# Performance work log

Measured on AMD Instinct MI355X. Metric: run time of the kernel, lower is better.

Reference implementation:

```python
import jax, jax.numpy as jnp
import numpy as np

D_MODEL = 1024
N_HEADS = 16
D_HEAD = D_MODEL // N_HEADS


def setup_inputs() -> dict:
    key = jax.random.key(0)
    ks = jax.random.split(key, 5)
    B, T = 2, 2048
    x = jax.random.normal(ks[0], (B, T, D_MODEL), dtype=jnp.float32)
    # Linear weights stored as [in, out]; scale ~ nn.Linear default magnitude
    W_qkv = jax.random.normal(ks[1], (D_MODEL, 3 * D_MODEL), dtype=jnp.float32) * (1.0 / np.sqrt(D_MODEL))
    b_qkv = jnp.zeros((3 * D_MODEL,), dtype=jnp.float32)
    W_out = jax.random.normal(ks[2], (D_MODEL, D_MODEL), dtype=jnp.float32) * (1.0 / np.sqrt(D_MODEL))
    b_out = jnp.zeros((D_MODEL,), dtype=jnp.float32)
    return {"x": x, "W_qkv": W_qkv, "b_qkv": b_qkv, "W_out": W_out, "b_out": b_out}


def reference(x, W_qkv, b_qkv, W_out, b_out):
    B, T, C = x.shape
    H, Dh = N_HEADS, D_HEAD
    qkv = x @ W_qkv + b_qkv                     # [B, T, 3C]
    q, k, v = jnp.split(qkv, 3, axis=-1)
    # [B, H, T, Dh]
    q = q.reshape(B, T, H, Dh).transpose(0, 2, 1, 3)
    k = k.reshape(B, T, H, Dh).transpose(0, 2, 1, 3)
    v = v.reshape(B, T, H, Dh).transpose(0, 2, 1, 3)
    att = jnp.einsum('bhqd,bhkd->bhqk', q, k) / np.sqrt(Dh).astype(np.float32)
    causal = jnp.tril(jnp.ones((T, T), dtype=bool))  # [T, T]
    att = jnp.where(causal[None, None], att, jnp.float32(-1e9))
    att = jax.nn.softmax(att, axis=-1)
    y = jnp.einsum('bhqk,bhkd->bhqd', att, v)   # [B, H, T, Dh]
    y = y.transpose(0, 2, 1, 3).reshape(B, T, C)
    y = y @ W_out + b_out
    return (y, k, v)  # y plus present KV cache
```

## Files before the change

kernel.cpp:

```cpp
#include <hip/hip_runtime.h>

typedef __attribute__((ext_vector_type(8))) short bf16x8;
typedef __attribute__((ext_vector_type(4))) float f32x4;
typedef __attribute__((ext_vector_type(16))) float f32x16;

#define MFMA16(A, B, C) __builtin_amdgcn_mfma_f32_16x16x32_bf16((A), (B), (C), 0, 0, 0)
#define MFMA32(A, B, C) __builtin_amdgcn_mfma_f32_32x32x16_bf16((A), (B), (C), 0, 0, 0)

union U8 { unsigned u[4]; bf16x8 v; };

__device__ __forceinline__ unsigned short f2b(float f) {
  unsigned u = __builtin_bit_cast(unsigned, f);
  unsigned r = (u + 0x7fffu + ((u >> 16) & 1u)) >> 16;
  return (unsigned short)r;
}

__device__ __forceinline__ unsigned cvtpk(float lo, float hi) {
  unsigned r;
  asm("v_cvt_pk_bf16_f32 %0, %1, %2" : "=v"(r) : "v"(lo), "v"(hi));
  return r;
}
__device__ __forceinline__ void swap32(unsigned& a, unsigned& b) {
  asm("v_permlane32_swap_b32 %0, %1" : "+v"(a), "+v"(b));
}

__device__ __forceinline__ void gload16(const void* g, void* l) {
  __builtin_amdgcn_global_load_lds(
      (const __attribute__((address_space(1))) void*)g,
      (__attribute__((address_space(3))) void*)l, 16, 0, 0);
}

__global__ void conv_bf16_kernel(const float* __restrict__ src,
                                 unsigned short* __restrict__ dst, int n) {
  int i = (blockIdx.x * blockDim.x + threadIdx.x) * 4;
  if (i < n) {
    float4 v = *(const float4*)(src + i);
    ushort4 o;
    o.x = f2b(v.x); o.y = f2b(v.y); o.z = f2b(v.z); o.w = f2b(v.w);
    *(ushort4*)(dst + i) = o;
  }
}

__global__ __launch_bounds__(1024) void transpose2_bf16_kernel(
    const float* __restrict__ s1, unsigned short* __restrict__ d1,
    const float* __restrict__ s2, unsigned short* __restrict__ d2) {
  __shared__ unsigned short t[32][33];
  int bx = (int)blockIdx.x;
  const float* src;
  unsigned short* dst;
  int C;
  if (bx < 96) { src = s1; dst = d1; C = 3072; }
  else         { src = s2; dst = d2; C = 1024; bx -= 96; }
  int x = threadIdx.x, y = threadIdx.y;
  int c0 = bx * 32, r0 = blockIdx.y * 32;
  t[y][x] = f2b(src[(size_t)(r0 + y) * C + c0 + x]);
  __syncthreads();
  dst[(size_t)(c0 + y) * 1024 + r0 + x] = t[x][y];
}

template <int MODE>
__global__ __launch_bounds__(256, 2) void gemm_bf16_kernel(
    const unsigned short* __restrict__ A, const unsigned short* __restrict__ Bt,
    const float* __restrict__ bias, int M, int N, int K,
    unsigned short* __restrict__ q_bf, unsigned short* __restrict__ k_bf,
    unsigned short* __restrict__ vt_bf, float* __restrict__ k_out,
    float* __restrict__ v_out, float* __restrict__ y_out) {
  __shared__ __align__(16) unsigned short As[128 * 64];
  __shared__ __align__(16) unsigned short Bs[128 * 64];
  const int tid = threadIdx.x;
  const int lane = tid & 63, wid = tid >> 6;
  const int wr = wid >> 1, wc = wid & 1;
  const int l15 = lane & 15, lg = lane >> 4;
  const int m0 = blockIdx.y * 128, n0 = blockIdx.x * 128;

  f32x4 acc[4][4] = {};

  int rowS[4], colS[4];
#pragma unroll
  for (int j = 0; j < 4; ++j) {
    int L = j * 4096 + wid * 1024 + lane * 16;
    int row = L >> 7;
    int c = (L & 127) ^ ((row & 7) << 4);
    rowS[j] = row;
    colS[j] = c >> 1;
  }

  for (int kt = 0; kt < K; kt += 64) {
    __syncthreads();
#pragma unroll
    for (int j = 0; j < 4; ++j) {
      gload16(A + (size_t)(m0 + rowS[j]) * K + kt + colS[j],
              (char*)As + j * 4096 + wid * 1024);
      gload16(Bt + (size_t)(n0 + rowS[j]) * K + kt + colS[j],
              (char*)Bs + j * 4096 + wid * 1024);
    }
    __syncthreads();

    bf16x8 af[4][2], bfr[4][2];
#pragma unroll
    for (int i = 0; i < 4; ++i)
#pragma unroll
      for (int kk = 0; kk < 2; ++kk) {
        int ra = wr * 64 + i * 16 + l15;
        int cb = kk * 64 + lg * 16;
        af[i][kk] = *(const bf16x8*)((const char*)As + ra * 128 + (cb ^ ((ra & 7) << 4)));
        int rb = wc * 64 + i * 16 + l15;
        bfr[i][kk] = *(const bf16x8*)((const char*)Bs + rb * 128 + (cb ^ ((rb & 7) << 4)));
      }
#pragma unroll
    for (int mi = 0; mi < 4; ++mi)
#pragma unroll
      for (int ni = 0; ni < 4; ++ni)
#pragma unroll
        for (int kk = 0; kk < 2; ++kk)
          acc[mi][ni] = MFMA16(af[mi][kk], bfr[ni][kk], acc[mi][ni]);
  }

#pragma unroll
  for (int ni = 0; ni < 4; ++ni) {
    int gn = n0 + wc * 64 + ni * 16 + l15;
    float bv = bias[gn];
    if (MODE == 0) {
      int which = gn >> 10, rem = gn & 1023;
      int h = rem >> 6, dh = rem & 63;
#pragma unroll
      for (int mi = 0; mi < 4; ++mi) {
        int gmb = m0 + wr * 64 + mi * 16 + lg * 4;
#pragma unroll
        for (int r = 0; r < 4; ++r) {
          int gm = gmb + r;
          int b = gm >> 11, t = gm & 2047;
          float val = acc[mi][ni][r] + bv;
          size_t idx = ((size_t)((b * 16 + h) * 2048 + t)) * 64 + dh;
          if (which == 0) {
            q_bf[idx] = f2b(val * 0.18033688f);
          } else if (which == 1) {
            k_out[idx] = val;
            k_bf[idx] = f2b(val);
          } else {
            v_out[idx] = val;
            vt_bf[((size_t)(b * 16 + h) * 64 + dh) * 2048 + t] = f2b(val);
          }
        }
      }
    } else {
#pragma unroll
      for (int mi = 0; mi < 4; ++mi) {
        int gmb = m0 + wr * 64 + mi * 16 + lg * 4;
#pragma unroll
        for (int r = 0; r < 4; ++r)
          y_out[(size_t)(gmb + r) * N + gn] = acc[mi][ni][r] + bv;
      }
    }
  }
}

__global__ __launch_bounds__(256, 2) void attn_kernel(
    const unsigned short* __restrict__ qbuf, const unsigned short* __restrict__ kb,
    const unsigned short* __restrict__ vtb, unsigned short* __restrict__ y_att) {
  __shared__ __align__(16) char lds_k[3][8192];
  __shared__ __align__(16) char lds_v[3][8192];
  const int tid = threadIdx.x, lane = tid & 63, w = tid >> 6;
  const int u = (int)blockIdx.x;
  const int bh = ((u & 7) << 2) | ((u >> 3) & 3);
  const int qb = 15 - (u >> 5);
  const int l31 = lane & 31, h = lane >> 5;
  const int qw0 = qb * 128 + w * 32;
  const size_t base_off = (size_t)bh * (2048 * 64);
  const unsigned short* Q = qbuf + base_off;
  const char* Kb = (const char*)(kb + base_off);
  const char* Vb = (const char*)(vtb + base_off);
  const int nt = 2 * qb + 2;
  const int my_last = (qw0 + 31) >> 6;

  int rowS[2], gcS[2];
#pragma unroll
  for (int j = 0; j < 2; ++j) {
    int L = tid * 16 + j * 4096;
    int row = L >> 7;
    rowS[j] = row;
    gcS[j] = (L & 127) ^ ((row & 7) << 4);
  }

#define STAGE(T, BUF)                                                           \
  if ((T) < nt) {                                                               \
    const int kv0_ = (T) * 64;                                                  \
    _Pragma("unroll") for (int j = 0; j < 2; ++j) {                             \
      gload16(Kb + (size_t)(kv0_ + rowS[j]) * 128 + gcS[j],                     \
              &lds_k[BUF][j * 4096 + tid * 16]);                                \
      gload16(Vb + (size_t)rowS[j] * 4096 + kv0_ * 2 + gcS[j],                  \
              &lds_v[BUF][j * 4096 + tid * 16]);                                \
    }                                                                           \
  }

  bf16x8 qB[4];
#pragma unroll
  for (int c = 0; c < 4; ++c)
    qB[c] = *(const bf16x8*)(Q + (size_t)(qw0 + l31) * 64 + c * 16 + h * 8);

  f32x16 yacc0 = {}, yacc1 = {};
  float m_run = -1e30f, l_run = 0.f;
  const int swz = (l31 & 7) << 4;

  STAGE(0, 0);
  STAGE(1, 1);

  int rs = 0;
  for (int t = 0; t < nt; ++t) {
    __syncthreads();
    const int wslot = rs < 1 ? rs + 2 : rs - 1;
    STAGE(t + 2, wslot);

    if (t <= my_last) {
      const char* Kl = lds_k[rs];
      const char* Vl = lds_v[rs];
      __builtin_amdgcn_s_setprio(1);
      f32x16 st0 = {}, st1 = {};
#pragma unroll
      for (int c = 0; c < 4; ++c) {
        bf16x8 k0 = *(const bf16x8*)(Kl + (size_t)l31 * 128 + ((c * 32 + h * 16) ^ swz));
        st0 = MFMA32(k0, qB[c], st0);
      }
#pragma unroll
      for (int c = 0; c < 4; ++c) {
        bf16x8 k1 = *(const bf16x8*)(Kl + (size_t)(32 + l31) * 128 + ((c * 32 + h * 16) ^ swz));
        st1 = MFMA32(k1, qB[c], st1);
      }
      __builtin_amdgcn_s_setprio(0);

      float s[32];
#pragma unroll
      for (int r = 0; r < 16; ++r) { s[r] = st0[r]; s[16 + r] = st1[r]; }
      if (t == my_last) {
#pragma unroll
        for (int r = 0; r < 32; ++r) {
          int key = t * 64 + (r >> 4) * 32 + (r & 3) + 8 * ((r >> 2) & 3) + 4 * h;
          if (key > qw0 + l31) s[r] = -1e30f;
        }
      }
      float tm[16];
#pragma unroll
      for (int r = 0; r < 16; ++r) tm[r] = fmaxf(s[r], s[r + 16]);
#pragma unroll
      for (int st_ = 8; st_ >= 1; st_ >>= 1)
#pragma unroll
        for (int r = 0; r < 8; ++r)
          if (r < st_) tm[r] = fmaxf(tm[r], tm[r + st_]);
      float mx = fmaxf(tm[0], __shfl_xor(tm[0], 32));
      if (__any(mx > m_run + 8.f)) {
        float mnew = fmaxf(m_run, mx);
        float alpha = exp2f(m_run - mnew);
#pragma unroll
        for (int r = 0; r < 16; ++r) { yacc0[r] *= alpha; yacc1[r] *= alpha; }
        l_run *= alpha;
        m_run = mnew;
      }
      float ls = 0.f;
#pragma unroll
      for (int r = 0; r < 32; ++r) {
        s[r] = exp2f(s[r] - m_run);
        ls += s[r];
      }
      ls += __shfl_xor(ls, 32);
      l_run += ls;

      U8 pf[4];
      {
        unsigned pk0 = cvtpk(s[0], s[1]), pk1 = cvtpk(s[2], s[3]);
        unsigned pk2 = cvtpk(s[4], s[5]), pk3 = cvtpk(s[6], s[7]);
        unsigned pk4 = cvtpk(s[8], s[9]), pk5 = cvtpk(s[10], s[11]);
        unsigned pk6 = cvtpk(s[12], s[13]), pk7 = cvtpk(s[14], s[15]);
        swap32(pk0, pk2); swap32(pk1, pk3); swap32(pk4, pk6); swap32(pk5, pk7);
        pf[0].u[0] = pk0; pf[0].u[1] = pk1; pf[0].u[2] = pk2; pf[0].u[3] = pk3;
        pf[1].u[0] = pk4; pf[1].u[1] = pk5; pf[1].u[2] = pk6; pf[1].u[3] = pk7;
        unsigned qk0 = cvtpk(s[16], s[17]), qk1 = cvtpk(s[18], s[19]);
        unsigned qk2 = cvtpk(s[20], s[21]), qk3 = cvtpk(s[22], s[23]);
        unsigned qk4 = cvtpk(s[24], s[25]), qk5 = cvtpk(s[26], s[27]);
        unsigned qk6 = cvtpk(s[28], s[29]), qk7 = cvtpk(s[30], s[31]);
        swap32(qk0, qk2); swap32(qk1, qk3); swap32(qk4, qk6); swap32(qk5, qk7);
        pf[2].u[0] = qk0; pf[2].u[1] = qk1; pf[2].u[2] = qk2; pf[2].u[3] = qk3;
        pf[3].u[0] = qk4; pf[3].u[1] = qk5; pf[3].u[2] = qk6; pf[3].u[3] = qk7;
      }

      __builtin_amdgcn_s_setprio(1);
#pragma unroll
      for (int c = 0; c < 4; ++c) {
        bf16x8 v0 = *(const bf16x8*)(Vl + (size_t)l31 * 128 + ((c * 32 + h * 16) ^ swz));
        yacc0 = MFMA32(v0, pf[c].v, yacc0);
      }
#pragma unroll
      for (int c = 0; c < 4; ++c) {
        bf16x8 v1 = *(const bf16x8*)(Vl + (size_t)(32 + l31) * 128 + ((c * 32 + h * 16) ^ swz));
        yacc1 = MFMA32(v1, pf[c].v, yacc1);
      }
      __builtin_amdgcn_s_setprio(0);
    }
    rs = rs < 2 ? rs + 1 : 0;
  }
#undef STAGE

  float inv = 1.f / l_run;
  const int b = bh >> 4, head = bh & 15;
  size_t rowb = ((size_t)(b * 2048 + qw0 + l31) * 16 + head) * 64;
#pragma unroll
  for (int rg = 0; rg < 4; ++rg) {
    int d0 = 8 * rg + 4 * h;
    ushort4 o0, o1;
    o0.x = f2b(yacc0[4 * rg + 0] * inv);
    o0.y = f2b(yacc0[4 * rg + 1] * inv);
    o0.z = f2b(yacc0[4 * rg + 2] * inv);
    o0.w = f2b(yacc0[4 * rg + 3] * inv);
    *(ushort4*)(y_att + rowb + d0) = o0;
    o1.x = f2b(yacc1[4 * rg + 0] * inv);
    o1.y = f2b(yacc1[4 * rg + 1] * inv);
    o1.z = f2b(yacc1[4 * rg + 2] * inv);
    o1.w = f2b(yacc1[4 * rg + 3] * inv);
    *(ushort4*)(y_att + rowb + 32 + d0) = o1;
  }
}

extern "C" void kernel_launch(void* const* d_in, const int* in_sizes, int n_in,
                              void* d_out, int out_size, void* d_ws, size_t ws_size,
                              hipStream_t stream) {
  const float* x = (const float*)d_in[0];
  const float* W_qkv = (const float*)d_in[1];
  const float* b_qkv = (const float*)d_in[2];
  const float* W_out = (const float*)d_in[3];
  const float* b_out = (const float*)d_in[4];

  float* y_out = (float*)d_out;
  float* k_out = y_out + 4194304;
  float* v_out = y_out + 8388608;

  unsigned short* x_bf = (unsigned short*)d_ws;
  unsigned short* wqkv_t = x_bf + 4194304;
  unsigned short* wout_t = wqkv_t + 3145728;
  unsigned short* q_bf = wout_t + 1048576;
  unsigned short* k_bf = q_bf + 4194304;
  unsigned short* vt_bf = k_bf + 4194304;
  unsigned short* y_att = vt_bf + 4194304;

  conv_bf16_kernel<<<4096, 256, 0, stream>>>(x, x_bf, 4194304);
  transpose2_bf16_kernel<<<dim3(128, 32), dim3(32, 32), 0, stream>>>(
      W_qkv, wqkv_t, W_out, wout_t);
  gemm_bf16_kernel<0><<<dim3(24, 32), 256, 0, stream>>>(
      x_bf, wqkv_t, b_qkv, 4096, 3072, 1024, q_bf, k_bf, vt_bf, k_out, v_out, nullptr);
  attn_kernel<<<512, 256, 0, stream>>>(q_bf, k_bf, vt_bf, y_att);
  gemm_bf16_kernel<1><<<dim3(8, 32), 256, 0, stream>>>(
      y_att, wout_t, b_out, 4096, 1024, 1024, nullptr, nullptr, nullptr, nullptr, nullptr, y_out);
}
```

Baseline: 135.5 us.

## Split long causal attention query blocks across two KV halves and merge

The longest causal query blocks (qb 8-15) are now split into two workgroups, each covering half of the KV range. Each half writes partial normalized outputs plus its running max and sum to scratch space reused from the x and weight buffers. A new merge kernel combines the two partials with log-sum-exp weights. This is meant to reduce tail imbalance and raise the number of workgroups from 512 to 768, at the cost of an extra launch, a bf16 round-trip of the partials, and some precision loss.

```diff
diff --git a/kernel.cpp b/kernel.cpp
--- a/kernel.cpp
+++ b/kernel.cpp
@@ -13,6 +13,10 @@
   unsigned u = __builtin_bit_cast(unsigned, f);
   unsigned r = (u + 0x7fffu + ((u >> 16) & 1u)) >> 16;
   return (unsigned short)r;
+}
+__device__ __forceinline__ float b2f(unsigned short u) {
+  unsigned v = ((unsigned)u) << 16;
+  return __builtin_bit_cast(float, v);
 }
 
 __device__ __forceinline__ unsigned cvtpk(float lo, float hi) {
@@ -157,20 +161,37 @@
 
 __global__ __launch_bounds__(256, 2) void attn_kernel(
     const unsigned short* __restrict__ qbuf, const unsigned short* __restrict__ kb,
-    const unsigned short* __restrict__ vtb, unsigned short* __restrict__ y_att) {
+    const unsigned short* __restrict__ vtb, unsigned short* __restrict__ y_att,
+    unsigned short* __restrict__ part_o, float2* __restrict__ part_ml) {
   __shared__ __align__(16) char lds_k[3][8192];
   __shared__ __align__(16) char lds_v[3][8192];
   const int tid = threadIdx.x, lane = tid & 63, w = tid >> 6;
   const int u = (int)blockIdx.x;
-  const int bh = ((u & 7) << 2) | ((u >> 3) & 3);
-  const int qb = 15 - (u >> 5);
+  int bh, qb, t0, t1, half, isplit;
+  if (u < 512) {
+    isplit = 1;
+    half = u & 1;
+    int w2 = u >> 1;
+    bh = w2 & 31;
+    qb = 15 - (w2 >> 5);
+    int ntf = 2 * qb + 2;
+    t0 = half ? 16 : 0;
+    t1 = half ? ntf : 16;
+  } else {
+    isplit = 0;
+    half = 0;
+    int s = u - 512;
+    bh = s & 31;
+    qb = 7 - (s >> 5);
+    t0 = 0;
+    t1 = 2 * qb + 2;
+  }
   const int l31 = lane & 31, h = lane >> 5;
   const int qw0 = qb * 128 + w * 32;
   const size_t base_off = (size_t)bh * (2048 * 64);
   const unsigned short* Q = qbuf + base_off;
   const char* Kb = (const char*)(kb + base_off);
   const char* Vb = (const char*)(vtb + base_off);
-  const int nt = 2 * qb + 2;
   const int my_last = (qw0 + 31) >> 6;
 
   int rowS[2], gcS[2];
@@ -183,7 +204,7 @@
   }
 
 #define STAGE(T, BUF)                                                           \
-  if ((T) < nt) {                                                               \
+  if ((T) < t1) {                                                               \
     const int kv0_ = (T) * 64;                                                  \
     _Pragma("unroll") for (int j = 0; j < 2; ++j) {                             \
       gload16(Kb + (size_t)(kv0_ + rowS[j]) * 128 + gcS[j],                     \
@@ -202,11 +223,11 @@
   float m_run = -1e30f, l_run = 0.f;
   const int swz = (l31 & 7) << 4;
 
-  STAGE(0, 0);
-  STAGE(1, 1);
+  STAGE(t0, 0);
+  STAGE(t0 + 1, 1);
 
   int rs = 0;
-  for (int t = 0; t < nt; ++t) {
+  for (int t = t0; t < t1; ++t) {
     __syncthreads();
     const int wslot = rs < 1 ? rs + 2 : rs - 1;
     STAGE(t + 2, wslot);
@@ -300,22 +321,80 @@
 #undef STAGE
 
   float inv = 1.f / l_run;
+  if (!isplit) {
+    const int b = bh >> 4, head = bh & 15;
+    size_t rowb = ((size_t)(b * 2048 + qw0 + l31) * 16 + head) * 64;
+#pragma unroll
+    for (int rg = 0; rg < 4; ++rg) {
+      int d0 = 8 * rg + 4 * h;
+      ushort4 o0, o1;
+      o0.x = f2b(yacc0[4 * rg + 0] * inv);
+      o0.y = f2b(yacc0[4 * rg + 1] * inv);
+      o0.z = f2b(yacc0[4 * rg + 2] * inv);
+      o0.w = f2b(yacc0[4 * rg + 3] * inv);
+      *(ushort4*)(y_att + rowb + d0) = o0;
+      o1.x = f2b(yacc1[4 * rg + 0] * inv);
+      o1.y = f2b(yacc1[4 * rg + 1] * inv);
+      o1.z = f2b(yacc1[4 * rg + 2] * inv);
+      o1.w = f2b(yacc1[4 * rg + 3] * inv);
+      *(ushort4*)(y_att + rowb + 32 + d0) = o1;
+    }
+  } else {
+    const int p = ((15 - qb) << 5) | bh;
+    unsigned short* po = part_o + (size_t)(p * 2 + half) * 8192;
+    const int lrow = w * 32 + l31;
+    size_t rowb = (size_t)lrow * 64;
+#pragma unroll
+    for (int rg = 0; rg < 4; ++rg) {
+      int d0 = 8 * rg + 4 * h;
+      ushort4 o0, o1;
+      o0.x = f2b(yacc0[4 * rg + 0] * inv);
+      o0.y = f2b(yacc0[4 * rg + 1] * inv);
+      o0.z = f2b(yacc0[4 * rg + 2] * inv);
+      o0.w = f2b(yacc0[4 * rg + 3] * inv);
+      *(ushort4*)(po + rowb + d0) = o0;
+      o1.x = f2b(yacc1[4 * rg + 0] * inv);
+      o1.y = f2b(yacc1[4 * rg + 1] * inv);
+      o1.z = f2b(yacc1[4 * rg + 2] * inv);
+      o1.w = f2b(yacc1[4 * rg + 3] * inv);
+      *(ushort4*)(po + rowb + 32 + d0) = o1;
+    }
+    if (h == 0) part_ml[(p * 2 + half) * 128 + lrow] = make_float2(m_run, l_run);
+  }
+}
+
+__global__ __launch_bounds__(256) void attn_merge_kernel(
+    const unsigned short* __restrict__ part_o, const float2* __restrict__ part_ml,
+    unsigned short* __restrict__ y_att) {
+  const int p = (int)blockIdx.x;
+  const int qb = 15 - (p >> 5);
+  const int bh = p & 31;
+  const int tid = threadIdx.x;
+  const int r = tid >> 1;
+  const int c0 = (tid & 1) << 5;
+  const unsigned short* o0 = part_o + (size_t)(p * 2 + 0) * 8192 + r * 64 + c0;
+  const unsigned short* o1 = part_o + (size_t)(p * 2 + 1) * 8192 + r * 64 + c0;
+  float2 ml0 = part_ml[(p * 2 + 0) * 128 + r];
+  float2 ml1 = part_ml[(p * 2 + 1) * 128 + r];
+  float mn = fmaxf(ml0.x, ml1.x);
+  float w0 = ml0.y * exp2f(ml0.x - mn);
+  float w1 = ml1.y * exp2f(ml1.x - mn);
+  float inv = 1.f / (w0 + w1);
+  w0 *= inv;
+  w1 *= inv;
   const int b = bh >> 4, head = bh & 15;
-  size_t rowb = ((size_t)(b * 2048 + qw0 + l31) * 16 + head) * 64;
-#pragma unroll
-  for (int rg = 0; rg < 4; ++rg) {
-    int d0 = 8 * rg + 4 * h;
-    ushort4 o0, o1;
-    o0.x = f2b(yacc0[4 * rg + 0] * inv);
-    o0.y = f2b(yacc0[4 * rg + 1] * inv);
-    o0.z = f2b(yacc0[4 * rg + 2] * inv);
-    o0.w = f2b(yacc0[4 * rg + 3] * inv);
-    *(ushort4*)(y_att + rowb + d0) = o0;
-    o1.x = f2b(yacc1[4 * rg + 0] * inv);
-    o1.y = f2b(yacc1[4 * rg + 1] * inv);
-    o1.z = f2b(yacc1[4 * rg + 2] * inv);
-    o1.w = f2b(yacc1[4 * rg + 3] * inv);
-    *(ushort4*)(y_att + rowb + 32 + d0) = o1;
+  unsigned short* dst =
+      y_att + ((size_t)(b * 2048 + qb * 128 + r) * 16 + head) * 64 + c0;
+#pragma unroll
+  for (int c = 0; c < 32; c += 4) {
+    ushort4 a = *(const ushort4*)(o0 + c);
+    ushort4 bb = *(const ushort4*)(o1 + c);
+    ushort4 o;
+    o.x = f2b(w0 * b2f(a.x) + w1 * b2f(bb.x));
+    o.y = f2b(w0 * b2f(a.y) + w1 * b2f(bb.y));
+    o.z = f2b(w0 * b2f(a.z) + w1 * b2f(bb.z));
+    o.w = f2b(w0 * b2f(a.w) + w1 * b2f(bb.w));
+    *(ushort4*)(dst + c) = o;
   }
 }
 
@@ -340,12 +419,16 @@
   unsigned short* vt_bf = k_bf + 4194304;
   unsigned short* y_att = vt_bf + 4194304;
 
+  unsigned short* part_o = x_bf;
+  float2* part_ml = (float2*)wqkv_t;
+
   conv_bf16_kernel<<<4096, 256, 0, stream>>>(x, x_bf, 4194304);
   transpose2_bf16_kernel<<<dim3(128, 32), dim3(32, 32), 0, stream>>>(
       W_qkv, wqkv_t, W_out, wout_t);
   gemm_bf16_kernel<0><<<dim3(24, 32), 256, 0, stream>>>(
       x_bf, wqkv_t, b_qkv, 4096, 3072, 1024, q_bf, k_bf, vt_bf, k_out, v_out, nullptr);
-  attn_kernel<<<512, 256, 0, stream>>>(q_bf, k_bf, vt_bf, y_att);
+  attn_kernel<<<768, 256, 0, stream>>>(q_bf, k_bf, vt_bf, y_att, part_o, part_ml);
+  attn_merge_kernel<<<256, 256, 0, stream>>>(part_o, part_ml, y_att);
   gemm_bf16_kernel<1><<<dim3(8, 32), 256, 0, stream>>>(
       y_att, wout_t, b_out, 4096, 1024, 1024, nullptr, nullptr, nullptr, nullptr, nullptr, y_out);
 }
```

Result: no change. 133.1 us (-1.8%).
